# Optimization experiments

Hardware: AMD Instinct MI355X
Metric: run time of the kernel (lower is better)

Reference implementation:

```python
import jax, jax.numpy as jnp
import numpy as np

NODE_DIM = 2
EMB_DIM = 128
SEQ_LEN = 5000
BATCH = 64


def _cyclic_positional_encoding(n_position, emb_dim, mean_pooling=True):
    """Faithful numpy port of EmbeddingNet.Cyclic_Positional_Encoding (init-time constant)."""
    Td_set = np.linspace(np.power(n_position, 1 / (emb_dim // 2)), n_position, emb_dim // 2, dtype='int')
    x = np.zeros((n_position, emb_dim))
    for i in range(emb_dim):
        Td = Td_set[i // 3 * 3 + 1] if i // 3 * 3 + 1 < emb_dim // 2 else Td_set[-1]
        fai = 0 if i <= emb_dim // 2 else 2 * np.pi * ((-i + emb_dim // 2) / (emb_dim // 2))
        longer = np.arange(0, np.ceil(n_position / Td) * Td, 0.01)
        idx = np.linspace(0, len(longer), n_position, dtype='int', endpoint=False)
        base = 2 * np.pi / Td * np.abs(np.mod(longer, 2 * Td) - Td) + fai
        x[:, i] = (np.cos(base) if i % 2 == 1 else np.sin(base))[idx]
    pat = x.astype(np.float32)
    ar = np.arange(n_position)
    shifts = [-2, -1, 0, 1, 2] if mean_pooling else [0]
    acc = np.zeros_like(pat)
    for s in shifts:
        acc += pat[(ar + s + n_position) % n_position]
    pat = acc / float(len(shifts)) - pat.mean(0)
    return jnp.asarray(pat, dtype=jnp.float32)


def setup_inputs() -> dict:
    key = jax.random.key(0)
    kx, kw, ks = jax.random.split(key, 3)
    x = jax.random.normal(kx, (BATCH, SEQ_LEN, NODE_DIM), dtype=jnp.float32)
    stdv = 1.0 / np.sqrt(NODE_DIM)
    W = jax.random.uniform(kw, (EMB_DIM, NODE_DIM), dtype=jnp.float32, minval=-stdv, maxval=stdv)
    pattern = _cyclic_positional_encoding(SEQ_LEN, EMB_DIM)  # [S, D]

    # solutions must be a single-cycle successor permutation over SEQ_LEN nodes
    def make_cycle(k):
        p = jax.random.permutation(k, SEQ_LEN)
        return jnp.zeros(SEQ_LEN, jnp.int32).at[p].set(jnp.roll(p, -1).astype(jnp.int32))

    solutions = jax.vmap(make_cycle)(jax.random.split(ks, BATCH))  # [B, S] int32
    return {"x": x, "W": W, "pattern": pattern, "solutions": solutions}


def reference(x, W, pattern, solutions):
    B, S = solutions.shape
    # pointer-chase: pre=0; visited_time[solutions[pre]] = i+1; pre = solutions[pre]
    def step(pre, _):
        nxt = jnp.take_along_axis(solutions, pre[:, None], axis=1)[:, 0]
        return nxt, nxt

    _, order = jax.lax.scan(step, jnp.zeros(B, dtype=solutions.dtype), None, length=S)
    order = order.T  # [B, S]: node visited at step i
    visited_time = jnp.zeros((B, S), jnp.int32).at[
        jnp.arange(B)[:, None], order
    ].set(jnp.arange(1, S + 1, dtype=jnp.int32)[None, :])
    idx = visited_time % S  # [B, S]
    PFEs = pattern[idx]  # gather -> [B, S, D]
    NFEs = jnp.einsum('bsn,dn->bsd', x, W)  # Linear(node_dim->emb, no bias)
    return NFEs, PFEs, visited_time
```

## Files before the change

kernel.cpp:

```cpp
#include <hip/hip_runtime.h>

#define SEQ 5000
#define BATCH 64
#define DIM 128

#define TPB1 1024
#define RANK_BLOCKS BATCH
#define NFE_BLOCKS 960
#define TPB2 512
#define PFE_BLOCKS 2048

typedef float f32x4 __attribute__((ext_vector_type(4)));

__global__ __launch_bounds__(TPB1) void rank_nfe_kernel(
    const float2* __restrict__ x,
    const f32x4* __restrict__ W,
    const int* __restrict__ sol,
    float* __restrict__ out) {
    __shared__ unsigned buf[2][SEQ];
    const size_t NFE = (size_t)BATCH * SEQ * DIM;

    if (blockIdx.x < RANK_BLOCKS) {
        const int b = blockIdx.x;
        const int* sp = sol + b * SEQ;
        float* vt_out = out + 2 * NFE;

        for (int i = threadIdx.x; i < SEQ; i += TPB1) {
            unsigned nx = (unsigned)sp[i];
            if (nx >= SEQ) nx = 0;
            buf[0][i] = (i == 0) ? 0u : ((1u << 16) | nx);
        }
        __syncthreads();
        int cur = 0;
#pragma unroll 1
        for (int it = 0; it < 13; ++it) {
            for (int i = threadIdx.x; i < SEQ; i += TPB1) {
                unsigned w  = buf[cur][i];
                unsigned w2 = buf[cur][w & 0xFFFFu];
                buf[cur ^ 1][i] = (w & 0xFFFF0000u) + w2;
            }
            __syncthreads();
            cur ^= 1;
        }
        for (int i = threadIdx.x; i < SEQ; i += TPB1) {
            int vt = SEQ - (int)(buf[cur][i] >> 16);
            vt_out[(size_t)b * SEQ + i] = (float)vt;
        }
    } else {
        f32x4* nfe4 = (f32x4*)out;
        const int c = threadIdx.x & 31;
        f32x4 wa = W[c * 2 + 0];
        f32x4 wb = W[c * 2 + 1];

        const size_t TOT = (size_t)BATCH * SEQ;
        const int ROWS = TPB1 / 32;
        for (size_t r = (size_t)(blockIdx.x - RANK_BLOCKS) * ROWS +
                        (threadIdx.x >> 5);
             r < TOT; r += (size_t)NFE_BLOCKS * ROWS) {
            float2 xv = x[r];
            f32x4 nv;
            nv.x = fmaf(xv.x, wa.x, xv.y * wa.y);
            nv.y = fmaf(xv.x, wa.z, xv.y * wa.w);
            nv.z = fmaf(xv.x, wb.x, xv.y * wb.y);
            nv.w = fmaf(xv.x, wb.z, xv.y * wb.w);
            __builtin_nontemporal_store(nv, &nfe4[r * 32 + c]);
        }
    }
}

__global__ __launch_bounds__(TPB2) void pfe_kernel(
    const f32x4* __restrict__ pat,
    const float* __restrict__ vt_in,
    float* __restrict__ out) {
    const size_t NFE = (size_t)BATCH * SEQ * DIM;
    f32x4* pfe4 = (f32x4*)(out + NFE);
    const int c = threadIdx.x & 31;

    const size_t TOT = (size_t)BATCH * SEQ;
    const int ROWS = TPB2 / 32;
    for (size_t r = (size_t)blockIdx.x * ROWS + (threadIdx.x >> 5);
         r < TOT; r += (size_t)PFE_BLOCKS * ROWS) {
        int vt = (int)vt_in[r];
        int i = (vt >= SEQ) ? 0 : vt;
        if ((unsigned)i >= SEQ) i = 0;
        f32x4 pv = pat[(size_t)i * 32 + c];
        __builtin_nontemporal_store(pv, &pfe4[r * 32 + c]);
    }
}

extern "C" void kernel_launch(void* const* d_in, const int* in_sizes, int n_in,
                              void* d_out, int out_size, void* d_ws, size_t ws_size,
                              hipStream_t stream) {
    const void* xp = d_in[0];
    const void* wp = d_in[1];
    const void* pp = d_in[2];
    const void* sp = d_in[3];
    {
        const void* big[2] = {nullptr, nullptr};
        int nbig = 0;
        const void *w_ = nullptr, *s_ = nullptr;
        for (int i = 0; i < n_in; ++i) {
            if (in_sizes[i] == DIM * 2) w_ = d_in[i];
            else if (in_sizes[i] == BATCH * SEQ) s_ = d_in[i];
            else if (in_sizes[i] == SEQ * DIM && nbig < 2) big[nbig++] = d_in[i];
        }
        if (w_ && s_ && nbig == 2) { wp = w_; sp = s_; xp = big[0]; pp = big[1]; }
    }

    const size_t NFE = (size_t)BATCH * SEQ * DIM;
    float* vt_region = (float*)d_out + 2 * NFE;

    rank_nfe_kernel<<<RANK_BLOCKS + NFE_BLOCKS, TPB1, 0, stream>>>(
        (const float2*)xp, (const f32x4*)wp, (const int*)sp, (float*)d_out);
    pfe_kernel<<<PFE_BLOCKS, TPB2, 0, stream>>>(
        (const f32x4*)pp, (const float*)vt_region, (float*)d_out);
}
```

Measured before the change: 334.8 us.

## Fuse rank, NFE and PFE stages into one cooperative kernel with grid sync

Merges the two launches into a single cooperative kernel of 512 blocks. Rank and NFE work run first, then a grid-wide sync, then every block does the PFE gather. The aim is to drop the second launch and the gap between kernels. In exchange there are fewer blocks, a grid barrier whose wait is set by the slow pointer-jumping rank blocks, and a fallback to the old two-kernel path if the cooperative launch fails.

```diff
diff --git a/kernel.cpp b/kernel.cpp
--- a/kernel.cpp
+++ b/kernel.cpp
@@ -1,30 +1,105 @@
 #include <hip/hip_runtime.h>
+#include <hip/hip_cooperative_groups.h>
+
+namespace cg = cooperative_groups;
 
 #define SEQ 5000
 #define BATCH 64
 #define DIM 128
 
-#define TPB1 1024
+#define COOP_TPB 1024
+#define COOP_BLOCKS 512
 #define RANK_BLOCKS BATCH
-#define NFE_BLOCKS 960
-#define TPB2 512
-#define PFE_BLOCKS 2048
 
 typedef float f32x4 __attribute__((ext_vector_type(4)));
 
-__global__ __launch_bounds__(TPB1) void rank_nfe_kernel(
+__global__ __launch_bounds__(COOP_TPB, 8) void fused_coop(
     const float2* __restrict__ x,
     const f32x4* __restrict__ W,
+    const f32x4* __restrict__ pat,
     const int* __restrict__ sol,
     float* __restrict__ out) {
     __shared__ unsigned buf[2][SEQ];
     const size_t NFE = (size_t)BATCH * SEQ * DIM;
+    const size_t TOT = (size_t)BATCH * SEQ;
+    const int c = threadIdx.x & 31;
 
     if (blockIdx.x < RANK_BLOCKS) {
         const int b = blockIdx.x;
         const int* sp = sol + b * SEQ;
         float* vt_out = out + 2 * NFE;
 
+        for (int i = threadIdx.x; i < SEQ; i += COOP_TPB) {
+            unsigned nx = (unsigned)sp[i];
+            if (nx >= SEQ) nx = 0;
+            buf[0][i] = (i == 0) ? 0u : ((1u << 16) | nx);
+        }
+        __syncthreads();
+        int cur = 0;
+#pragma unroll 1
+        for (int it = 0; it < 13; ++it) {
+            for (int i = threadIdx.x; i < SEQ; i += COOP_TPB) {
+                unsigned w  = buf[cur][i];
+                unsigned w2 = buf[cur][w & 0xFFFFu];
+                buf[cur ^ 1][i] = (w & 0xFFFF0000u) + w2;
+            }
+            __syncthreads();
+            cur ^= 1;
+        }
+        for (int i = threadIdx.x; i < SEQ; i += COOP_TPB) {
+            int vt = SEQ - (int)(buf[cur][i] >> 16);
+            vt_out[(size_t)b * SEQ + i] = (float)vt;
+        }
+    } else {
+        f32x4* nfe4 = (f32x4*)out;
+        f32x4 wa = W[c * 2 + 0];
+        f32x4 wb = W[c * 2 + 1];
+        const int ROWS = COOP_TPB / 32;
+        for (size_t r = (size_t)(blockIdx.x - RANK_BLOCKS) * ROWS +
+                        (threadIdx.x >> 5);
+             r < TOT; r += (size_t)(COOP_BLOCKS - RANK_BLOCKS) * ROWS) {
+            float2 xv = x[r];
+            f32x4 nv;
+            nv.x = fmaf(xv.x, wa.x, xv.y * wa.y);
+            nv.y = fmaf(xv.x, wa.z, xv.y * wa.w);
+            nv.z = fmaf(xv.x, wb.x, xv.y * wb.y);
+            nv.w = fmaf(xv.x, wb.z, xv.y * wb.w);
+            __builtin_nontemporal_store(nv, &nfe4[r * 32 + c]);
+        }
+    }
+
+    __threadfence();
+    cg::this_grid().sync();
+
+    {
+        f32x4* pfe4 = (f32x4*)(out + NFE);
+        const float* vt_in = out + 2 * NFE;
+        const int ROWS = COOP_TPB / 32;
+        for (size_t r = (size_t)blockIdx.x * ROWS + (threadIdx.x >> 5);
+             r < TOT; r += (size_t)COOP_BLOCKS * ROWS) {
+            int vt = (int)vt_in[r];
+            int i = (vt >= SEQ) ? 0 : vt;
+            if ((unsigned)i >= SEQ) i = 0;
+            f32x4 pv = pat[(size_t)i * 32 + c];
+            __builtin_nontemporal_store(pv, &pfe4[r * 32 + c]);
+        }
+    }
+}
+
+#define TPB1 1024
+#define NFE_BLOCKS 960
+#define TPB2 512
+#define PFE_BLOCKS 2048
+
+__global__ __launch_bounds__(TPB1) void rank_nfe_kernel(
+    const float2* __restrict__ x, const f32x4* __restrict__ W,
+    const int* __restrict__ sol, float* __restrict__ out) {
+    __shared__ unsigned buf[2][SEQ];
+    const size_t NFE = (size_t)BATCH * SEQ * DIM;
+    if (blockIdx.x < RANK_BLOCKS) {
+        const int b = blockIdx.x;
+        const int* sp = sol + b * SEQ;
+        float* vt_out = out + 2 * NFE;
         for (int i = threadIdx.x; i < SEQ; i += TPB1) {
             unsigned nx = (unsigned)sp[i];
             if (nx >= SEQ) nx = 0;
@@ -51,7 +126,6 @@
         const int c = threadIdx.x & 31;
         f32x4 wa = W[c * 2 + 0];
         f32x4 wb = W[c * 2 + 1];
-
         const size_t TOT = (size_t)BATCH * SEQ;
         const int ROWS = TPB1 / 32;
         for (size_t r = (size_t)(blockIdx.x - RANK_BLOCKS) * ROWS +
@@ -69,13 +143,11 @@
 }
 
 __global__ __launch_bounds__(TPB2) void pfe_kernel(
-    const f32x4* __restrict__ pat,
-    const float* __restrict__ vt_in,
+    const f32x4* __restrict__ pat, const float* __restrict__ vt_in,
     float* __restrict__ out) {
     const size_t NFE = (size_t)BATCH * SEQ * DIM;
     f32x4* pfe4 = (f32x4*)(out + NFE);
     const int c = threadIdx.x & 31;
-
     const size_t TOT = (size_t)BATCH * SEQ;
     const int ROWS = TPB2 / 32;
     for (size_t r = (size_t)blockIdx.x * ROWS + (threadIdx.x >> 5);
@@ -107,11 +179,23 @@
         if (w_ && s_ && nbig == 2) { wp = w_; sp = s_; xp = big[0]; pp = big[1]; }
     }
 
-    const size_t NFE = (size_t)BATCH * SEQ * DIM;
-    float* vt_region = (float*)d_out + 2 * NFE;
-
-    rank_nfe_kernel<<<RANK_BLOCKS + NFE_BLOCKS, TPB1, 0, stream>>>(
-        (const float2*)xp, (const f32x4*)wp, (const int*)sp, (float*)d_out);
-    pfe_kernel<<<PFE_BLOCKS, TPB2, 0, stream>>>(
-        (const f32x4*)pp, (const float*)vt_region, (float*)d_out);
-}
+    const float2* xa = (const float2*)xp;
+    const f32x4*  wa = (const f32x4*)wp;
+    const f32x4*  pa = (const f32x4*)pp;
+    const int*    sa = (const int*)sp;
+    float*        oa = (float*)d_out;
+
+    void* args[] = {(void*)&xa, (void*)&wa, (void*)&pa, (void*)&sa, (void*)&oa};
+    hipError_t e = hipLaunchCooperativeKernel(
+        (const void*)fused_coop, dim3(COOP_BLOCKS), dim3(COOP_TPB),
+        args, 0, stream);
+
+    if (e != hipSuccess) {
+        (void)hipGetLastError();
+        const size_t NFE = (size_t)BATCH * SEQ * DIM;
+        float* vt_region = (float*)d_out + 2 * NFE;
+        rank_nfe_kernel<<<RANK_BLOCKS + NFE_BLOCKS, TPB1, 0, stream>>>(
+            xa, wa, sa, oa);
+        pfe_kernel<<<PFE_BLOCKS, TPB2, 0, stream>>>(pa, vt_region, oa);
+    }
+}
```

After: 617.7 us. 84.5% more time.
